# Optimization experiments

Measured on AMD Instinct MI355X. Metric: run time of the kernel, lower is better.

The kernel has to match this reference:

```python
import jax, jax.numpy as jnp
import numpy as np


def setup_inputs() -> dict:
    key = jax.random.key(0)
    k1, k2 = jax.random.split(key)
    B, T, D, K = 16, 4096, 1024, 512
    h = jax.random.normal(k1, (B, T, D), dtype=jnp.float32)
    codebook = jax.random.normal(k2, (K, D), dtype=jnp.float32)
    return {"h": h, "codebook": codebook}


def reference(h, codebook):
    """SAMMCodebook.encode: nearest-codeword indices via squared L2 distance.

    h: [B, T, D]; codebook: [K, D] -> z: [B, T] int32
    """
    B, T, D = h.shape
    h_flat = h.reshape(-1, D)                                  # [N, D]
    h_sq = jnp.sum(h_flat * h_flat, axis=-1, keepdims=True)    # [N, 1]
    c_sq = jnp.sum(codebook * codebook, axis=-1)[None, :]      # [1, K]
    # dist[n,k] = ||h_n||^2 + ||c_k||^2 - 2 <h_n, c_k>
    dist = h_sq + c_sq - 2.0 * (h_flat @ codebook.T)           # [N, K]
    z = jnp.argmin(dist, axis=-1).reshape(B, T)
    return z.astype(jnp.int32)
```

## Files before the change

### kernel.cpp

```cpp
#include <hip/hip_runtime.h>


#define D_DIM 1024
#define K_CB  512
#define BM    64
#define BN    256
#define BK    64
#define STRIDE 72
#define DELTA 4.0f
#define SENTINEL 0x7FFF

typedef __attribute__((ext_vector_type(8))) short short8;
typedef __attribute__((ext_vector_type(4))) float floatx4;

static __device__ __forceinline__ unsigned short f2bf(float f) {
    unsigned u = __builtin_bit_cast(unsigned, f);
    unsigned r = (u + 0x7FFFu + ((u >> 16) & 1u)) >> 16;
    return (unsigned short)r;
}

__global__ __launch_bounds__(256)
void prep_kernel(const float* __restrict__ cb, unsigned short* __restrict__ cbb,
                 float* __restrict__ csq) {
    __shared__ float red[4];
    const int k = blockIdx.x, t = threadIdx.x;
    const float4 v = *(const float4*)(cb + (size_t)k * D_DIM + t * 4);
    uint2 u;
    u.x = (unsigned)f2bf(v.x) | ((unsigned)f2bf(v.y) << 16);
    u.y = (unsigned)f2bf(v.z) | ((unsigned)f2bf(v.w) << 16);
    *(uint2*)(cbb + (size_t)k * D_DIM + t * 4) = u;
    float s = v.x * v.x + v.y * v.y + v.z * v.z + v.w * v.w;
    #pragma unroll
    for (int off = 32; off > 0; off >>= 1) s += __shfl_down(s, off, 64);
    if ((t & 63) == 0) red[t >> 6] = s;
    __syncthreads();
    if (t == 0) csq[k] = red[0] + red[1] + red[2] + red[3];
}

__global__ __launch_bounds__(256)
void coarse_kernel(const float* __restrict__ h,
                   const unsigned short* __restrict__ cbb,
                   const float* __restrict__ csq,
                   uint4* __restrict__ slots) {
    __shared__ unsigned char smem[46080] __attribute__((aligned(16)));
    unsigned short* hs = (unsigned short*)smem;
    unsigned short* cs = (unsigned short*)(smem + 64 * STRIDE * 2);

    const int tid = threadIdx.x;
    const int w = tid >> 6;
    const int lane = tid & 63;
    const int l15 = lane & 15;
    const int kq = lane >> 4;

    const int rowblk = blockIdx.x >> 1;
    const int half = blockIdx.x & 1;
    const size_t row0 = (size_t)rowblk * BM;
    const int col0 = half * BN;

    const int wr = (w >> 1) * 32;
    const int wc = (w & 1) * 128;

    floatx4 acc[2][8];
    #pragma unroll
    for (int i = 0; i < 2; ++i)
        #pragma unroll
        for (int j = 0; j < 8; ++j) acc[i][j] = (floatx4){0.f, 0.f, 0.f, 0.f};

    for (int dk = 0; dk < D_DIM; dk += BK) {
        #pragma unroll
        for (int p = 0; p < 4; ++p) {
            const int f = p * 256 + tid;
            const int r = f >> 4, c4 = f & 15;
            const float4 v = *(const float4*)(h + (row0 + r) * D_DIM + dk + c4 * 4);
            uint2 u;
            u.x = (unsigned)f2bf(v.x) | ((unsigned)f2bf(v.y) << 16);
            u.y = (unsigned)f2bf(v.z) | ((unsigned)f2bf(v.w) << 16);
            *(uint2*)(hs + r * STRIDE + c4 * 4) = u;
        }
        #pragma unroll
        for (int p = 0; p < 8; ++p) {
            const int f = p * 256 + tid;
            const int cr = f >> 3, g = f & 7;
            const uint4 u = *(const uint4*)(cbb + (size_t)(col0 + cr) * D_DIM + dk + g * 8);
            *(uint4*)(cs + cr * STRIDE + g * 8) = u;
        }
        __syncthreads();
        #pragma unroll
        for (int ks = 0; ks < BK; ks += 32) {
            short8 a[2], b[8];
            #pragma unroll
            for (int rt = 0; rt < 2; ++rt)
                a[rt] = *(const short8*)(hs + (wr + rt * 16 + l15) * STRIDE + ks + kq * 8);
            #pragma unroll
            for (int ct = 0; ct < 8; ++ct)
                b[ct] = *(const short8*)(cs + (wc + ct * 16 + l15) * STRIDE + ks + kq * 8);
            #pragma unroll
            for (int rt = 0; rt < 2; ++rt)
                #pragma unroll
                for (int ct = 0; ct < 8; ++ct)
                    acc[rt][ct] = __builtin_amdgcn_mfma_f32_16x16x32_bf16(
                        a[rt], b[ct], acc[rt][ct], 0, 0, 0);
        }
        __syncthreads();
    }

    float k1[8], k2[8];
    int   c1[8], c2[8];
    #pragma unroll
    for (int i = 0; i < 8; ++i) { k1[i] = 3.4e38f; k2[i] = 3.4e38f; c1[i] = 0; c2[i] = 0; }

    #pragma unroll
    for (int ct = 0; ct < 8; ++ct) {
        const int col = col0 + wc + ct * 16 + l15;
        const float cq = csq[col];
        #pragma unroll
        for (int rt = 0; rt < 2; ++rt)
            #pragma unroll
            for (int reg = 0; reg < 4; ++reg) {
                const float s = fmaf(-2.0f, acc[rt][ct][reg], cq);
                const int ri = rt * 4 + reg;
                if (s < k1[ri]) { k2[ri] = k1[ri]; c2[ri] = c1[ri]; k1[ri] = s; c1[ri] = col; }
                else if (s < k2[ri]) { k2[ri] = s; c2[ri] = col; }
            }
    }

    float* mval = (float*)smem;
    int*   mcol = (int*)(smem + 64 * 66 * 4);
    __syncthreads();
    #pragma unroll
    for (int rt = 0; rt < 2; ++rt)
        #pragma unroll
        for (int reg = 0; reg < 4; ++reg) {
            const int ri = rt * 4 + reg;
            const int r = wr + rt * 16 + kq * 4 + reg;
            const int e = ((w & 1) * 16 + l15) * 2;
            mval[r * 66 + e] = k1[ri];     mcol[r * 66 + e] = c1[ri];
            mval[r * 66 + e + 1] = k2[ri]; mcol[r * 66 + e + 1] = c2[ri];
        }
    __syncthreads();

    if (tid < 64) {
        const int r = tid;
        float bv = 3.4e38f; int bc = 0x7fffffff;
        for (int e = 0; e < 64; ++e) {
            const float v = mval[r * 66 + e];
            const int   c = mcol[r * 66 + e];
            if (v < bv || (v == bv && c < bc)) { bv = v; bc = c; }
        }
        const float thr = bv + DELTA;
        unsigned cd[4] = {0, 0, 0, 0};
        int others = 0;
        for (int e = 0; e < 64; ++e) {
            const float v = mval[r * 66 + e];
            const int   c = mcol[r * 66 + e];
            if (v < thr && c != bc) {
                if (others < 4) cd[others] = (unsigned)c;
                ++others;
            }
        }
        unsigned cnt = (others > 4) ? (unsigned)SENTINEL : (unsigned)(1 + others);
        uint4 s;
        s.x = __builtin_bit_cast(unsigned, bv);
        s.y = (unsigned)bc | (cnt << 16);
        s.z = cd[0] | (cd[1] << 16);
        s.w = cd[2] | (cd[3] << 16);
        slots[(row0 + r) * 2 + half] = s;
    }
}

__global__ __launch_bounds__(256)
void refine_kernel(const float* __restrict__ h, const float* __restrict__ cb,
                   const float* __restrict__ csq, const uint4* __restrict__ slots,
                   int* __restrict__ out) {
    const int w = threadIdx.x >> 6;
    const int lane = threadIdx.x & 63;
    const size_t row = (size_t)blockIdx.x * 4 + w;

    const uint4 s0 = slots[row * 2 + 0];
    const uint4 s1 = slots[row * 2 + 1];
    const float bv0 = __builtin_bit_cast(float, s0.x);
    const float bv1 = __builtin_bit_cast(float, s1.x);
    const float gmin = fminf(bv0, bv1);
    const float thr = gmin + DELTA;

    int cl[10];
    int nc = 0;
    bool full = false;
    {
        const uint4 ss[2] = {s0, s1};
        const float bvh[2] = {bv0, bv1};
        for (int hh = 0; hh < 2; ++hh) {
            if (!(bvh[hh] < thr)) continue;
            const unsigned cnt = ss[hh].y >> 16;
            if (cnt == SENTINEL) { full = true; continue; }
            cl[nc++] = (int)(ss[hh].y & 0xFFFFu);
            const unsigned cds[4] = {ss[hh].z & 0xFFFFu, ss[hh].z >> 16,
                                     ss[hh].w & 0xFFFFu, ss[hh].w >> 16};
            for (unsigned i = 0; i + 1 < cnt; ++i) cl[nc++] = (int)cds[i];
        }
    }

    if (!full && nc == 1) {
        if (lane == 0) out[row] = cl[0];
        return;
    }

    const float* hrow = h + row * D_DIM;
    float4 hv[4];
    #pragma unroll
    for (int j = 0; j < 4; ++j)
        hv[j] = *(const float4*)(hrow + j * 256 + lane * 4);

    float bs = 3.4e38f; int bc = 0x7fffffff;
    const int total = full ? K_CB : nc;
    for (int i = 0; i < total; ++i) {
        const int c = full ? i : cl[i];
        const float* crow = cb + (size_t)c * D_DIM;
        float d = 0.0f;
        #pragma unroll
        for (int j = 0; j < 4; ++j) {
            const float4 cv = *(const float4*)(crow + j * 256 + lane * 4);
            d = fmaf(hv[j].x, cv.x, d);
            d = fmaf(hv[j].y, cv.y, d);
            d = fmaf(hv[j].z, cv.z, d);
            d = fmaf(hv[j].w, cv.w, d);
        }
        #pragma unroll
        for (int off = 32; off > 0; off >>= 1) d += __shfl_down(d, off, 64);
        d = __shfl(d, 0, 64);
        const float s = fmaf(-2.0f, d, csq[c]);
        if (s < bs || (s == bs && c < bc)) { bs = s; bc = c; }
    }
    if (lane == 0) out[row] = bc;
}

extern "C" void kernel_launch(void* const* d_in, const int* in_sizes, int n_in,
                              void* d_out, int out_size, void* d_ws, size_t ws_size,
                              hipStream_t stream) {
    const float* h  = (const float*)d_in[0];
    const float* cb = (const float*)d_in[1];
    int* out = (int*)d_out;

    unsigned char* ws = (unsigned char*)d_ws;
    unsigned short* cbb = (unsigned short*)ws;
    float* csq = (float*)(ws + 1048576);
    uint4* slots = (uint4*)(ws + 1048576 + 2048);

    const int nrows = in_sizes[0] / D_DIM;

    prep_kernel<<<dim3(K_CB), dim3(256), 0, stream>>>(cb, cbb, csq);
    coarse_kernel<<<dim3((nrows / BM) * 2), dim3(256), 0, stream>>>(h, cbb, csq, slots);
    refine_kernel<<<dim3(nrows / 4), dim3(256), 0, stream>>>(h, cb, csq, slots, out);
}
```

Before: 486.1 us.

## Pre-convert h to bf16, async LDS-load GEMM over full codebook, worklist refine

```diff
diff --git a/kernel.cpp b/kernel.cpp
--- a/kernel.cpp
+++ b/kernel.cpp
@@ -3,20 +3,42 @@
 
 #define D_DIM 1024
 #define K_CB  512
-#define BM    64
-#define BN    256
-#define BK    64
-#define STRIDE 72
 #define DELTA 4.0f
-#define SENTINEL 0x7FFF
+#define SENTINEL 0x7FFFu
 
 typedef __attribute__((ext_vector_type(8))) short short8;
 typedef __attribute__((ext_vector_type(4))) float floatx4;
 
-static __device__ __forceinline__ unsigned short f2bf(float f) {
+#define WS_HB    0ull
+#define WS_CBB   134217728ull
+#define WS_CSQ   135266304ull
+#define WS_SLOT  135268352ull
+#define WS_WL    136316928ull
+#define WS_CNT   136579072ull
+#define WS_NEED  136579136ull
+
+typedef const unsigned int __attribute__((address_space(1)))* gaddr_t;
+typedef unsigned int __attribute__((address_space(3)))* laddr_t;
+static __device__ __forceinline__ void async_copy16(const void* g, void* l) {
+    __builtin_amdgcn_global_load_lds((gaddr_t)g, (laddr_t)l, 16, 0, 0);
+}
+
+static __device__ __forceinline__ unsigned f2bf(float f) {
     unsigned u = __builtin_bit_cast(unsigned, f);
-    unsigned r = (u + 0x7FFFu + ((u >> 16) & 1u)) >> 16;
-    return (unsigned short)r;
+    return (u + 0x7FFFu + ((u >> 16) & 1u)) >> 16;
+}
+
+__global__ __launch_bounds__(256)
+void hconv_kernel(const float* __restrict__ h, unsigned short* __restrict__ hb) {
+    const size_t i = ((size_t)blockIdx.x * 256 + threadIdx.x) * 8;
+    const float4 v0 = *(const float4*)(h + i);
+    const float4 v1 = *(const float4*)(h + i + 4);
+    uint4 u;
+    u.x = f2bf(v0.x) | (f2bf(v0.y) << 16);
+    u.y = f2bf(v0.z) | (f2bf(v0.w) << 16);
+    u.z = f2bf(v1.x) | (f2bf(v1.y) << 16);
+    u.w = f2bf(v1.z) | (f2bf(v1.w) << 16);
+    *(uint4*)(hb + i) = u;
 }
 
 __global__ __launch_bounds__(256)
@@ -26,8 +48,8 @@
     const int k = blockIdx.x, t = threadIdx.x;
     const float4 v = *(const float4*)(cb + (size_t)k * D_DIM + t * 4);
     uint2 u;
-    u.x = (unsigned)f2bf(v.x) | ((unsigned)f2bf(v.y) << 16);
-    u.y = (unsigned)f2bf(v.z) | ((unsigned)f2bf(v.w) << 16);
+    u.x = f2bf(v.x) | (f2bf(v.y) << 16);
+    u.y = f2bf(v.z) | (f2bf(v.w) << 16);
     *(uint2*)(cbb + (size_t)k * D_DIM + t * 4) = u;
     float s = v.x * v.x + v.y * v.y + v.z * v.z + v.w * v.w;
     #pragma unroll
@@ -37,6 +59,202 @@
     if (t == 0) csq[k] = red[0] + red[1] + red[2] + red[3];
 }
 
+__global__ __launch_bounds__(256, 2)
+void coarse2_kernel(const unsigned short* __restrict__ hb,
+                    const unsigned short* __restrict__ cbb,
+                    const float* __restrict__ csq,
+                    uint4* __restrict__ slots,
+                    int* __restrict__ wl,
+                    unsigned* __restrict__ wcount,
+                    int* __restrict__ out) {
+    __shared__ unsigned char smem[33792] __attribute__((aligned(16)));
+    unsigned short* As = (unsigned short*)smem;
+    unsigned short* Bs = (unsigned short*)(smem + 8192);
+
+    const int tid = threadIdx.x;
+    const int w = tid >> 6, lane = tid & 63;
+    const int l15 = lane & 15, kq = lane >> 4;
+    const int wr = (w >> 1) * 64, wc = (w & 1) * 64;
+    const size_t row0 = (size_t)blockIdx.x * 128;
+
+    int rS[2], qS[2];
+    #pragma unroll
+    for (int j = 0; j < 2; ++j) {
+        const int slot = j * 256 + w * 64 + lane;
+        rS[j] = slot >> 2; qS[j] = slot & 3;
+    }
+    const unsigned short* gA[2];
+    #pragma unroll
+    for (int j = 0; j < 2; ++j)
+        gA[j] = hb + (row0 + rS[j]) * D_DIM + qS[j] * 8;
+
+    float k1[16], k2[16];
+    unsigned cpk[16];
+    #pragma unroll
+    for (int i = 0; i < 16; ++i) { k1[i] = 3.4e38f; k2[i] = 3.4e38f; cpk[i] = 0; }
+
+    for (int cc = 0; cc < 4; ++cc) {
+        floatx4 acc[4][4];
+        #pragma unroll
+        for (int i = 0; i < 4; ++i)
+            #pragma unroll
+            for (int j = 0; j < 4; ++j) acc[i][j] = (floatx4){0.f, 0.f, 0.f, 0.f};
+
+        const unsigned short* gB[2];
+        #pragma unroll
+        for (int j = 0; j < 2; ++j)
+            gB[j] = cbb + (size_t)(cc * 128 + rS[j]) * D_DIM + qS[j] * 8;
+
+        #pragma unroll 2
+        for (int dk = 0; dk < D_DIM; dk += 32) {
+            #pragma unroll
+            for (int j = 0; j < 2; ++j) {
+                const size_t lds_off = (size_t)(j * 256 + w * 64) * 8;
+                async_copy16(gA[j] + dk, As + lds_off);
+                async_copy16(gB[j] + dk, Bs + lds_off);
+            }
+            __syncthreads();
+            short8 a[4], b[4];
+            #pragma unroll
+            for (int rt = 0; rt < 4; ++rt)
+                a[rt] = *(const short8*)(As + (wr + rt * 16 + l15) * 32 + kq * 8);
+            #pragma unroll
+            for (int ct = 0; ct < 4; ++ct)
+                b[ct] = *(const short8*)(Bs + (wc + ct * 16 + l15) * 32 + kq * 8);
+            #pragma unroll
+            for (int rt = 0; rt < 4; ++rt)
+                #pragma unroll
+                for (int ct = 0; ct < 4; ++ct)
+                    acc[rt][ct] = __builtin_amdgcn_mfma_f32_16x16x32_bf16(
+                        a[rt], b[ct], acc[rt][ct], 0, 0, 0);
+            __syncthreads();
+        }
+
+        #pragma unroll
+        for (int ct = 0; ct < 4; ++ct) {
+            const int col = cc * 128 + wc + ct * 16 + l15;
+            const float cq = csq[col];
+            #pragma unroll
+            for (int rt = 0; rt < 4; ++rt)
+                #pragma unroll
+                for (int reg = 0; reg < 4; ++reg) {
+                    const float s = fmaf(-2.0f, acc[rt][ct][reg], cq);
+                    const int ri = rt * 4 + reg;
+                    if (s < k1[ri]) {
+                        k2[ri] = k1[ri]; k1[ri] = s;
+                        cpk[ri] = (cpk[ri] << 16) | (unsigned)col;
+                    } else if (s < k2[ri]) {
+                        k2[ri] = s;
+                        cpk[ri] = (cpk[ri] & 0xFFFFu) | ((unsigned)col << 16);
+                    }
+                }
+        }
+    }
+
+    float* mval = (float*)smem;
+    int*   mcol = (int*)(smem + 16896);
+    for (int p = 0; p < 2; ++p) {
+        __syncthreads();
+        if ((w >> 1) == p) {
+            #pragma unroll
+            for (int rt = 0; rt < 4; ++rt)
+                #pragma unroll
+                for (int reg = 0; reg < 4; ++reg) {
+                    const int ri = rt * 4 + reg;
+                    const int rl = rt * 16 + kq * 4 + reg;
+                    const int e = ((w & 1) * 16 + l15) * 2;
+                    mval[rl * 66 + e] = k1[ri];
+                    mcol[rl * 66 + e] = (int)(cpk[ri] & 0xFFFFu);
+                    mval[rl * 66 + e + 1] = k2[ri];
+                    mcol[rl * 66 + e + 1] = (int)(cpk[ri] >> 16);
+                }
+        }
+        __syncthreads();
+        if (tid < 64) {
+            const int r = tid;
+            float bv = mval[r * 66]; int bc = mcol[r * 66];
+            for (int e = 1; e < 64; ++e) {
+                const float v = mval[r * 66 + e];
+                const int   c = mcol[r * 66 + e];
+                if (v < bv || (v == bv && c < bc)) { bv = v; bc = c; }
+            }
+            const float thr = bv + DELTA;
+            unsigned cd[4] = {0, 0, 0, 0};
+            int others = 0;
+            for (int e = 0; e < 64; ++e) {
+                const float v = mval[r * 66 + e];
+                const int   c = mcol[r * 66 + e];
+                if (v < thr && c != bc) {
+                    if (others < 4) cd[others] = (unsigned)c;
+                    ++others;
+                }
+            }
+            const size_t grow = row0 + (size_t)p * 64 + r;
+            if (others == 0) {
+                out[grow] = bc;
+            } else {
+                const unsigned cnt = (others > 4) ? SENTINEL : (unsigned)(1 + others);
+                uint4 s;
+                s.x = __builtin_bit_cast(unsigned, bv);
+                s.y = (unsigned)bc | (cnt << 16);
+                s.z = cd[0] | (cd[1] << 16);
+                s.w = cd[2] | (cd[3] << 16);
+                slots[grow] = s;
+                wl[atomicAdd(wcount, 1u)] = (int)grow;
+            }
+        }
+    }
+}
+
+__global__ __launch_bounds__(256)
+void refine2_kernel(const float* __restrict__ h, const float* __restrict__ cb,
+                    const float* __restrict__ csq, const uint4* __restrict__ slots,
+                    const int* __restrict__ wl, const unsigned* __restrict__ wcount,
+                    int* __restrict__ out) {
+    const int w = threadIdx.x >> 6, lane = threadIdx.x & 63;
+    const unsigned total = *wcount;
+    for (unsigned idx = blockIdx.x * 4 + w; idx < total; idx += 1024) {
+        const size_t row = (size_t)wl[idx];
+        const uint4 s = slots[row];
+        const unsigned cnt = s.y >> 16;
+        const bool full = (cnt == SENTINEL);
+        int cl[5]; int nc = 0;
+        if (!full) {
+            nc = (int)cnt;
+            cl[0] = (int)(s.y & 0xFFFFu);
+            const unsigned cds[4] = {s.z & 0xFFFFu, s.z >> 16, s.w & 0xFFFFu, s.w >> 16};
+            for (int i = 1; i < nc; ++i) cl[i] = (int)cds[i - 1];
+        }
+        const float* hrow = h + row * D_DIM;
+        float4 hv[4];
+        #pragma unroll
+        for (int j = 0; j < 4; ++j)
+            hv[j] = *(const float4*)(hrow + j * 256 + lane * 4);
+        float bs = 3.4e38f; int bc = 0x7fffffff;
+        const int tot = full ? K_CB : nc;
+        for (int i = 0; i < tot; ++i) {
+            const int c = full ? i : cl[i];
+            const float* crow = cb + (size_t)c * D_DIM;
+            float d = 0.0f;
+            #pragma unroll
+            for (int j = 0; j < 4; ++j) {
+                const float4 cv = *(const float4*)(crow + j * 256 + lane * 4);
+                d = fmaf(hv[j].x, cv.x, d);
+                d = fmaf(hv[j].y, cv.y, d);
+                d = fmaf(hv[j].z, cv.z, d);
+                d = fmaf(hv[j].w, cv.w, d);
+            }
+            #pragma unroll
+            for (int off = 32; off > 0; off >>= 1) d += __shfl_down(d, off, 64);
+            d = __shfl(d, 0, 64);
+            const float sc = fmaf(-2.0f, d, csq[c]);
+            if (sc < bs || (sc == bs && c < bc)) { bs = sc; bc = c; }
+        }
+        if (lane == 0) out[row] = bc;
+    }
+}
+
+#define STRIDE 72
 __global__ __launch_bounds__(256)
 void coarse_kernel(const float* __restrict__ h,
                    const unsigned short* __restrict__ cbb,
@@ -45,36 +263,27 @@
     __shared__ unsigned char smem[46080] __attribute__((aligned(16)));
     unsigned short* hs = (unsigned short*)smem;
     unsigned short* cs = (unsigned short*)(smem + 64 * STRIDE * 2);
-
     const int tid = threadIdx.x;
-    const int w = tid >> 6;
-    const int lane = tid & 63;
-    const int l15 = lane & 15;
-    const int kq = lane >> 4;
-
-    const int rowblk = blockIdx.x >> 1;
-    const int half = blockIdx.x & 1;
-    const size_t row0 = (size_t)rowblk * BM;
-    const int col0 = half * BN;
-
-    const int wr = (w >> 1) * 32;
-    const int wc = (w & 1) * 128;
-
+    const int w = tid >> 6, lane = tid & 63;
+    const int l15 = lane & 15, kq = lane >> 4;
+    const int rowblk = blockIdx.x >> 1, half = blockIdx.x & 1;
+    const size_t row0 = (size_t)rowblk * 64;
+    const int col0 = half * 256;
+    const int wr = (w >> 1) * 32, wc = (w & 1) * 128;
     floatx4 acc[2][8];
     #pragma unroll
     for (int i = 0; i < 2; ++i)
         #pragma unroll
         for (int j = 0; j < 8; ++j) acc[i][j] = (floatx4){0.f, 0.f, 0.f, 0.f};
-
-    for (int dk = 0; dk < D_DIM; dk += BK) {
+    for (int dk = 0; dk < D_DIM; dk += 64) {
         #pragma unroll
         for (int p = 0; p < 4; ++p) {
             const int f = p * 256 + tid;
             const int r = f >> 4, c4 = f & 15;
             const float4 v = *(const float4*)(h + (row0 + r) * D_DIM + dk + c4 * 4);
             uint2 u;
-            u.x = (unsigned)f2bf(v.x) | ((unsigned)f2bf(v.y) << 16);
-            u.y = (unsigned)f2bf(v.z) | ((unsigned)f2bf(v.w) << 16);
+            u.x = f2bf(v.x) | (f2bf(v.y) << 16);
+            u.y = f2bf(v.z) | (f2bf(v.w) << 16);
             *(uint2*)(hs + r * STRIDE + c4 * 4) = u;
         }
         #pragma unroll
@@ -86,7 +295,7 @@
         }
         __syncthreads();
         #pragma unroll
-        for (int ks = 0; ks < BK; ks += 32) {
+        for (int ks = 0; ks < 64; ks += 32) {
             short8 a[2], b[8];
             #pragma unroll
             for (int rt = 0; rt < 2; ++rt)
@@ -103,12 +312,9 @@
         }
         __syncthreads();
     }
-
-    float k1[8], k2[8];
-    int   c1[8], c2[8];
+    float k1[8], k2[8]; int c1[8], c2[8];
     #pragma unroll
     for (int i = 0; i < 8; ++i) { k1[i] = 3.4e38f; k2[i] = 3.4e38f; c1[i] = 0; c2[i] = 0; }
-
     #pragma unroll
     for (int ct = 0; ct < 8; ++ct) {
         const int col = col0 + wc + ct * 16 + l15;
@@ -123,7 +329,6 @@
                 else if (s < k2[ri]) { k2[ri] = s; c2[ri] = col; }
             }
     }
-
     float* mval = (float*)smem;
     int*   mcol = (int*)(smem + 64 * 66 * 4);
     __syncthreads();
@@ -138,7 +343,6 @@
             mval[r * 66 + e + 1] = k2[ri]; mcol[r * 66 + e + 1] = c2[ri];
         }
     __syncthreads();
-
     if (tid < 64) {
         const int r = tid;
         float bv = 3.4e38f; int bc = 0x7fffffff;
@@ -158,7 +362,7 @@
                 ++others;
             }
         }
-        unsigned cnt = (others > 4) ? (unsigned)SENTINEL : (unsigned)(1 + others);
+        unsigned cnt = (others > 4) ? SENTINEL : (unsigned)(1 + others);
         uint4 s;
         s.x = __builtin_bit_cast(unsigned, bv);
         s.y = (unsigned)bc | (cnt << 16);
@@ -172,20 +376,14 @@
 void refine_kernel(const float* __restrict__ h, const float* __restrict__ cb,
                    const float* __restrict__ csq, const uint4* __restrict__ slots,
                    int* __restrict__ out) {
-    const int w = threadIdx.x >> 6;
-    const int lane = threadIdx.x & 63;
+    const int w = threadIdx.x >> 6, lane = threadIdx.x & 63;
     const size_t row = (size_t)blockIdx.x * 4 + w;
-
     const uint4 s0 = slots[row * 2 + 0];
     const uint4 s1 = slots[row * 2 + 1];
     const float bv0 = __builtin_bit_cast(float, s0.x);
     const float bv1 = __builtin_bit_cast(float, s1.x);
-    const float gmin = fminf(bv0, bv1);
-    const float thr = gmin + DELTA;
-
-    int cl[10];
-    int nc = 0;
-    bool full = false;
+    const float thr = fminf(bv0, bv1) + DELTA;
+    int cl[10]; int nc = 0; bool full = false;
     {
         const uint4 ss[2] = {s0, s1};
         const float bvh[2] = {bv0, bv1};
@@ -199,18 +397,11 @@
             for (unsigned i = 0; i + 1 < cnt; ++i) cl[nc++] = (int)cds[i];
         }
     }
-
-    if (!full && nc == 1) {
-        if (lane == 0) out[row] = cl[0];
-        return;
-    }
-
+    if (!full && nc == 1) { if (lane == 0) out[row] = cl[0]; return; }
     const float* hrow = h + row * D_DIM;
     float4 hv[4];
     #pragma unroll
-    for (int j = 0; j < 4; ++j)
-        hv[j] = *(const float4*)(hrow + j * 256 + lane * 4);
-
+    for (int j = 0; j < 4; ++j) hv[j] = *(const float4*)(hrow + j * 256 + lane * 4);
     float bs = 3.4e38f; int bc = 0x7fffffff;
     const int total = full ? K_CB : nc;
     for (int i = 0; i < total; ++i) {
@@ -228,8 +419,8 @@
         #pragma unroll
         for (int off = 32; off > 0; off >>= 1) d += __shfl_down(d, off, 64);
         d = __shfl(d, 0, 64);
-        const float s = fmaf(-2.0f, d, csq[c]);
-        if (s < bs || (s == bs && c < bc)) { bs = s; bc = c; }
+        const float sc = fmaf(-2.0f, d, csq[c]);
+        if (sc < bs || (sc == bs && c < bc)) { bs = sc; bc = c; }
     }
     if (lane == 0) out[row] = bc;
 }
@@ -240,15 +431,29 @@
     const float* h  = (const float*)d_in[0];
     const float* cb = (const float*)d_in[1];
     int* out = (int*)d_out;
-
     unsigned char* ws = (unsigned char*)d_ws;
-    unsigned short* cbb = (unsigned short*)ws;
-    float* csq = (float*)(ws + 1048576);
-    uint4* slots = (uint4*)(ws + 1048576 + 2048);
-
     const int nrows = in_sizes[0] / D_DIM;
 
-    prep_kernel<<<dim3(K_CB), dim3(256), 0, stream>>>(cb, cbb, csq);
-    coarse_kernel<<<dim3((nrows / BM) * 2), dim3(256), 0, stream>>>(h, cbb, csq, slots);
-    refine_kernel<<<dim3(nrows / 4), dim3(256), 0, stream>>>(h, cb, csq, slots, out);
-}
+    if (ws_size >= WS_NEED) {
+        unsigned short* hb  = (unsigned short*)(ws + WS_HB);
+        unsigned short* cbb = (unsigned short*)(ws + WS_CBB);
+        float* csq   = (float*)(ws + WS_CSQ);
+        uint4* slots = (uint4*)(ws + WS_SLOT);
+        int*   wl    = (int*)(ws + WS_WL);
+        unsigned* wc = (unsigned*)(ws + WS_CNT);
+        hipMemsetAsync(wc, 0, 4, stream);
+        hconv_kernel<<<dim3((nrows * (D_DIM / 8)) / 256), dim3(256), 0, stream>>>(h, hb);
+        prep_kernel<<<dim3(K_CB), dim3(256), 0, stream>>>(cb, cbb, csq);
+        coarse2_kernel<<<dim3(nrows / 128), dim3(256), 0, stream>>>(
+            hb, cbb, csq, slots, wl, wc, out);
+        refine2_kernel<<<dim3(256), dim3(256), 0, stream>>>(
+            h, cb, csq, slots, wl, wc, out);
+    } else {
+        unsigned short* cbb = (unsigned short*)ws;
+        float* csq   = (float*)(ws + 1048576);
+        uint4* slots = (uint4*)(ws + 1048576 + 2048);
+        prep_kernel<<<dim3(K_CB), dim3(256), 0, stream>>>(cb, cbb, csq);
+        coarse_kernel<<<dim3((nrows / 64) * 2), dim3(256), 0, stream>>>(h, cbb, csq, slots);
+        refine_kernel<<<dim3(nrows / 4), dim3(256), 0, stream>>>(h, cb, csq, slots, out);
+    }
+}
```

Result: slower. 880.6 us (+81.2%).

## Cover full codebook per block, async-load B, and compact refine worklist

Applied to the files above, without the earlier changes.

```diff
diff --git a/kernel.cpp b/kernel.cpp
--- a/kernel.cpp
+++ b/kernel.cpp
@@ -3,20 +3,28 @@
 
 #define D_DIM 1024
 #define K_CB  512
-#define BM    64
-#define BN    256
-#define BK    64
-#define STRIDE 72
 #define DELTA 4.0f
-#define SENTINEL 0x7FFF
+#define MAXC  8
+#define SENT  0xFFFFu
 
 typedef __attribute__((ext_vector_type(8))) short short8;
 typedef __attribute__((ext_vector_type(4))) float floatx4;
 
-static __device__ __forceinline__ unsigned short f2bf(float f) {
+#define WS_CBB  0ull
+#define WS_CSQ  1048576ull
+#define WS_SLOT 1050624ull
+#define WS_WL   3147776ull
+#define WS_CNT  3409920ull
+
+typedef const unsigned int __attribute__((address_space(1)))* gaddr_t;
+typedef unsigned int __attribute__((address_space(3)))* laddr_t;
+static __device__ __forceinline__ void async_copy16(const void* g, void* l) {
+    __builtin_amdgcn_global_load_lds((gaddr_t)g, (laddr_t)l, 16, 0, 0);
+}
+
+static __device__ __forceinline__ unsigned f2bf(float f) {
     unsigned u = __builtin_bit_cast(unsigned, f);
-    unsigned r = (u + 0x7FFFu + ((u >> 16) & 1u)) >> 16;
-    return (unsigned short)r;
+    return (u + 0x7FFFu + ((u >> 16) & 1u)) >> 16;
 }
 
 __global__ __launch_bounds__(256)
@@ -26,8 +34,8 @@
     const int k = blockIdx.x, t = threadIdx.x;
     const float4 v = *(const float4*)(cb + (size_t)k * D_DIM + t * 4);
     uint2 u;
-    u.x = (unsigned)f2bf(v.x) | ((unsigned)f2bf(v.y) << 16);
-    u.y = (unsigned)f2bf(v.z) | ((unsigned)f2bf(v.w) << 16);
+    u.x = f2bf(v.x) | (f2bf(v.y) << 16);
+    u.y = f2bf(v.z) | (f2bf(v.w) << 16);
     *(uint2*)(cbb + (size_t)k * D_DIM + t * 4) = u;
     float s = v.x * v.x + v.y * v.y + v.z * v.z + v.w * v.w;
     #pragma unroll
@@ -37,172 +45,168 @@
     if (t == 0) csq[k] = red[0] + red[1] + red[2] + red[3];
 }
 
-__global__ __launch_bounds__(256)
+__global__ __launch_bounds__(256, 2)
 void coarse_kernel(const float* __restrict__ h,
                    const unsigned short* __restrict__ cbb,
                    const float* __restrict__ csq,
-                   uint4* __restrict__ slots) {
-    __shared__ unsigned char smem[46080] __attribute__((aligned(16)));
-    unsigned short* hs = (unsigned short*)smem;
-    unsigned short* cs = (unsigned short*)(smem + 64 * STRIDE * 2);
+                   uint4* __restrict__ slots,
+                   int* __restrict__ wl,
+                   unsigned* __restrict__ wcount,
+                   int* __restrict__ out) {
+    __shared__ unsigned char smem[66560] __attribute__((aligned(16)));
+    unsigned short* As = (unsigned short*)smem;
+    unsigned short* Bs = (unsigned short*)(smem + 4096);
 
     const int tid = threadIdx.x;
-    const int w = tid >> 6;
-    const int lane = tid & 63;
-    const int l15 = lane & 15;
-    const int kq = lane >> 4;
-
-    const int rowblk = blockIdx.x >> 1;
-    const int half = blockIdx.x & 1;
-    const size_t row0 = (size_t)rowblk * BM;
-    const int col0 = half * BN;
-
-    const int wr = (w >> 1) * 32;
-    const int wc = (w & 1) * 128;
-
-    floatx4 acc[2][8];
-    #pragma unroll
-    for (int i = 0; i < 2; ++i)
+    const int w = tid >> 6, lane = tid & 63;
+    const int l15 = lane & 15, kq = lane >> 4;
+    const size_t row0 = (size_t)blockIdx.x * 64;
+    const int wc_ = w * 128;
+
+    const int ar = tid >> 2, adq = (tid & 3) * 8;
+    const float* gA = h + (row0 + ar) * D_DIM + adq;
+    const unsigned short* gB0 = cbb + (size_t)(tid >> 2) * D_DIM + (tid & 3) * 8;
+    unsigned short* ldsB0 = Bs + (size_t)(w * 64 + (lane)) * 0;
+
+    floatx4 acc[4][8];
+    #pragma unroll
+    for (int i = 0; i < 4; ++i)
         #pragma unroll
         for (int j = 0; j < 8; ++j) acc[i][j] = (floatx4){0.f, 0.f, 0.f, 0.f};
 
-    for (int dk = 0; dk < D_DIM; dk += BK) {
-        #pragma unroll
-        for (int p = 0; p < 4; ++p) {
-            const int f = p * 256 + tid;
-            const int r = f >> 4, c4 = f & 15;
-            const float4 v = *(const float4*)(h + (row0 + r) * D_DIM + dk + c4 * 4);
-            uint2 u;
-            u.x = (unsigned)f2bf(v.x) | ((unsigned)f2bf(v.y) << 16);
-            u.y = (unsigned)f2bf(v.z) | ((unsigned)f2bf(v.w) << 16);
-            *(uint2*)(hs + r * STRIDE + c4 * 4) = u;
-        }
-        #pragma unroll
-        for (int p = 0; p < 8; ++p) {
-            const int f = p * 256 + tid;
-            const int cr = f >> 3, g = f & 7;
-            const uint4 u = *(const uint4*)(cbb + (size_t)(col0 + cr) * D_DIM + dk + g * 8);
-            *(uint4*)(cs + cr * STRIDE + g * 8) = u;
-        }
+    for (int dk = 0; dk < D_DIM; dk += 32) {
+        #pragma unroll
+        for (int j = 0; j < 8; ++j)
+            async_copy16(gB0 + (size_t)j * 64 * D_DIM + dk,
+                         Bs + (size_t)(j * 256 + w * 64) * 8);
+        const float4 v0 = *(const float4*)(gA + dk);
+        const float4 v1 = *(const float4*)(gA + dk + 4);
+        uint4 u;
+        u.x = f2bf(v0.x) | (f2bf(v0.y) << 16);
+        u.y = f2bf(v0.z) | (f2bf(v0.w) << 16);
+        u.z = f2bf(v1.x) | (f2bf(v1.y) << 16);
+        u.w = f2bf(v1.z) | (f2bf(v1.w) << 16);
+        *(uint4*)(As + ar * 32 + adq) = u;
         __syncthreads();
-        #pragma unroll
-        for (int ks = 0; ks < BK; ks += 32) {
-            short8 a[2], b[8];
-            #pragma unroll
-            for (int rt = 0; rt < 2; ++rt)
-                a[rt] = *(const short8*)(hs + (wr + rt * 16 + l15) * STRIDE + ks + kq * 8);
+
+        short8 a[4], b[8];
+        #pragma unroll
+        for (int rt = 0; rt < 4; ++rt)
+            a[rt] = *(const short8*)(As + (rt * 16 + l15) * 32 + kq * 8);
+        #pragma unroll
+        for (int ct = 0; ct < 8; ++ct)
+            b[ct] = *(const short8*)(Bs + (wc_ + ct * 16 + l15) * 32 + kq * 8);
+        #pragma unroll
+        for (int rt = 0; rt < 4; ++rt)
             #pragma unroll
             for (int ct = 0; ct < 8; ++ct)
-                b[ct] = *(const short8*)(cs + (wc + ct * 16 + l15) * STRIDE + ks + kq * 8);
-            #pragma unroll
-            for (int rt = 0; rt < 2; ++rt)
-                #pragma unroll
-                for (int ct = 0; ct < 8; ++ct)
-                    acc[rt][ct] = __builtin_amdgcn_mfma_f32_16x16x32_bf16(
-                        a[rt], b[ct], acc[rt][ct], 0, 0, 0);
-        }
+                acc[rt][ct] = __builtin_amdgcn_mfma_f32_16x16x32_bf16(
+                    a[rt], b[ct], acc[rt][ct], 0, 0, 0);
         __syncthreads();
     }
 
-    float k1[8], k2[8];
-    int   c1[8], c2[8];
-    #pragma unroll
-    for (int i = 0; i < 8; ++i) { k1[i] = 3.4e38f; k2[i] = 3.4e38f; c1[i] = 0; c2[i] = 0; }
-
+    float k1[16], k2[16];
+    unsigned cpk[16];
+    #pragma unroll
+    for (int i = 0; i < 16; ++i) { k1[i] = 3.4e38f; k2[i] = 3.4e38f; cpk[i] = 0; }
     #pragma unroll
     for (int ct = 0; ct < 8; ++ct) {
-        const int col = col0 + wc + ct * 16 + l15;
+        const int col = wc_ + ct * 16 + l15;
         const float cq = csq[col];
         #pragma unroll
-        for (int rt = 0; rt < 2; ++rt)
+        for (int rt = 0; rt < 4; ++rt)
             #pragma unroll
             for (int reg = 0; reg < 4; ++reg) {
                 const float s = fmaf(-2.0f, acc[rt][ct][reg], cq);
                 const int ri = rt * 4 + reg;
-                if (s < k1[ri]) { k2[ri] = k1[ri]; c2[ri] = c1[ri]; k1[ri] = s; c1[ri] = col; }
-                else if (s < k2[ri]) { k2[ri] = s; c2[ri] = col; }
+                if (s < k1[ri]) {
+                    k2[ri] = k1[ri]; k1[ri] = s;
+                    cpk[ri] = (cpk[ri] << 16) | (unsigned)col;
+                } else if (s < k2[ri]) {
+                    k2[ri] = s;
+                    cpk[ri] = (cpk[ri] & 0xFFFFu) | ((unsigned)col << 16);
+                }
             }
     }
 
     float* mval = (float*)smem;
-    int*   mcol = (int*)(smem + 64 * 66 * 4);
+    int*   mcol = (int*)(smem + 33280);
     __syncthreads();
     #pragma unroll
-    for (int rt = 0; rt < 2; ++rt)
+    for (int rt = 0; rt < 4; ++rt)
         #pragma unroll
         for (int reg = 0; reg < 4; ++reg) {
             const int ri = rt * 4 + reg;
-            const int r = wr + rt * 16 + kq * 4 + reg;
-            const int e = ((w & 1) * 16 + l15) * 2;
-            mval[r * 66 + e] = k1[ri];     mcol[r * 66 + e] = c1[ri];
-            mval[r * 66 + e + 1] = k2[ri]; mcol[r * 66 + e + 1] = c2[ri];
+            const int r = rt * 16 + kq * 4 + reg;
+            const int e = (w * 16 + l15) * 2;
+            mval[r * 130 + e] = k1[ri];
+            mcol[r * 130 + e] = (int)(cpk[ri] & 0xFFFFu);
+            mval[r * 130 + e + 1] = k2[ri];
+            mcol[r * 130 + e + 1] = (int)(cpk[ri] >> 16);
         }
     __syncthreads();
 
     if (tid < 64) {
         const int r = tid;
-        float bv = 3.4e38f; int bc = 0x7fffffff;
-        for (int e = 0; e < 64; ++e) {
-            const float v = mval[r * 66 + e];
-            const int   c = mcol[r * 66 + e];
+        float bv = mval[r * 130]; int bc = mcol[r * 130];
+        for (int e = 1; e < 128; ++e) {
+            const float v = mval[r * 130 + e];
+            const int   c = mcol[r * 130 + e];
             if (v < bv || (v == bv && c < bc)) { bv = v; bc = c; }
         }
         const float thr = bv + DELTA;
-        unsigned cd[4] = {0, 0, 0, 0};
+        unsigned cd[MAXC] = {0, 0, 0, 0, 0, 0, 0, 0};
         int others = 0;
-        for (int e = 0; e < 64; ++e) {
-            const float v = mval[r * 66 + e];
-            const int   c = mcol[r * 66 + e];
+        for (int e = 0; e < 128; ++e) {
+            const float v = mval[r * 130 + e];
+            const int   c = mcol[r * 130 + e];
             if (v < thr && c != bc) {
-                if (others < 4) cd[others] = (unsigned)c;
+                if (others < MAXC) cd[others] = (unsigned)c;
                 ++others;
             }
         }
-        unsigned cnt = (others > 4) ? (unsigned)SENTINEL : (unsigned)(1 + others);
-        uint4 s;
-        s.x = __builtin_bit_cast(unsigned, bv);
-        s.y = (unsigned)bc | (cnt << 16);
-        s.z = cd[0] | (cd[1] << 16);
-        s.w = cd[2] | (cd[3] << 16);
-        slots[(row0 + r) * 2 + half] = s;
+        const size_t grow = row0 + r;
+        if (others == 0) {
+            out[grow] = bc;
+        } else {
+            const unsigned cnt = (others > MAXC) ? SENT : (unsigned)others;
+            uint4 s0, s1;
+            s0.x = __builtin_bit_cast(unsigned, bv);
+            s0.y = (unsigned)bc | (cnt << 16);
+            s0.z = cd[0] | (cd[1] << 16);
+            s0.w = cd[2] | (cd[3] << 16);
+            s1.x = cd[4] | (cd[5] << 16);
+            s1.y = cd[6] | (cd[7] << 16);
+            s1.z = 0; s1.w = 0;
+            slots[grow * 2] = s0;
+            slots[grow * 2 + 1] = s1;
+            wl[atomicAdd(wcount, 1u)] = (int)grow;
+        }
     }
 }
 
 __global__ __launch_bounds__(256)
-void refine_kernel(const float* __restrict__ h, const float* __restrict__ cb,
-                   const float* __restrict__ csq, const uint4* __restrict__ slots,
-                   int* __restrict__ out) {
-    const int w = threadIdx.x >> 6;
-    const int lane = threadIdx.x & 63;
-    const size_t row = (size_t)blockIdx.x * 4 + w;
-
-    const uint4 s0 = slots[row * 2 + 0];
+void fixup_kernel(const float* __restrict__ h, const float* __restrict__ cb,
+                  const float* __restrict__ csq, const uint4* __restrict__ slots,
+                  const int* __restrict__ wl, const unsigned* __restrict__ wcount,
+                  int* __restrict__ out) {
+    const int w = threadIdx.x >> 6, lane = threadIdx.x & 63;
+    const unsigned idx = blockIdx.x * 4 + w;
+    if (idx >= *wcount) return;
+    const size_t row = (size_t)wl[idx];
+    const uint4 s0 = slots[row * 2];
     const uint4 s1 = slots[row * 2 + 1];
-    const float bv0 = __builtin_bit_cast(float, s0.x);
-    const float bv1 = __builtin_bit_cast(float, s1.x);
-    const float gmin = fminf(bv0, bv1);
-    const float thr = gmin + DELTA;
-
-    int cl[10];
-    int nc = 0;
-    bool full = false;
-    {
-        const uint4 ss[2] = {s0, s1};
-        const float bvh[2] = {bv0, bv1};
-        for (int hh = 0; hh < 2; ++hh) {
-            if (!(bvh[hh] < thr)) continue;
-            const unsigned cnt = ss[hh].y >> 16;
-            if (cnt == SENTINEL) { full = true; continue; }
-            cl[nc++] = (int)(ss[hh].y & 0xFFFFu);
-            const unsigned cds[4] = {ss[hh].z & 0xFFFFu, ss[hh].z >> 16,
-                                     ss[hh].w & 0xFFFFu, ss[hh].w >> 16};
-            for (unsigned i = 0; i + 1 < cnt; ++i) cl[nc++] = (int)cds[i];
-        }
-    }
-
-    if (!full && nc == 1) {
-        if (lane == 0) out[row] = cl[0];
-        return;
+    const unsigned cnt = s0.y >> 16;
+    const bool full = (cnt == SENT);
+    int cl[1 + MAXC]; int nc = 0;
+    if (!full) {
+        cl[0] = (int)(s0.y & 0xFFFFu);
+        const unsigned cds[MAXC] = {s0.z & 0xFFFFu, s0.z >> 16, s0.w & 0xFFFFu, s0.w >> 16,
+                                    s1.x & 0xFFFFu, s1.x >> 16, s1.y & 0xFFFFu, s1.y >> 16};
+        nc = 1 + (int)cnt;
+        #pragma unroll
+        for (int i = 0; i < MAXC; ++i)
+            if (i < (int)cnt) cl[1 + i] = (int)cds[i];
     }
 
     const float* hrow = h + row * D_DIM;
@@ -228,8 +232,8 @@
         #pragma unroll
         for (int off = 32; off > 0; off >>= 1) d += __shfl_down(d, off, 64);
         d = __shfl(d, 0, 64);
-        const float s = fmaf(-2.0f, d, csq[c]);
-        if (s < bs || (s == bs && c < bc)) { bs = s; bc = c; }
+        const float sc = fmaf(-2.0f, d, csq[c]);
+        if (sc < bs || (sc == bs && c < bc)) { bs = sc; bc = c; }
     }
     if (lane == 0) out[row] = bc;
 }
@@ -240,15 +244,19 @@
     const float* h  = (const float*)d_in[0];
     const float* cb = (const float*)d_in[1];
     int* out = (int*)d_out;
-
     unsigned char* ws = (unsigned char*)d_ws;
-    unsigned short* cbb = (unsigned short*)ws;
-    float* csq = (float*)(ws + 1048576);
-    uint4* slots = (uint4*)(ws + 1048576 + 2048);
-
     const int nrows = in_sizes[0] / D_DIM;
 
+    unsigned short* cbb = (unsigned short*)(ws + WS_CBB);
+    float* csq   = (float*)(ws + WS_CSQ);
+    uint4* slots = (uint4*)(ws + WS_SLOT);
+    int*   wl    = (int*)(ws + WS_WL);
+    unsigned* wc = (unsigned*)(ws + WS_CNT);
+
+    hipMemsetAsync(wc, 0, 4, stream);
     prep_kernel<<<dim3(K_CB), dim3(256), 0, stream>>>(cb, cbb, csq);
-    coarse_kernel<<<dim3((nrows / BM) * 2), dim3(256), 0, stream>>>(h, cbb, csq, slots);
-    refine_kernel<<<dim3(nrows / 4), dim3(256), 0, stream>>>(h, cb, csq, slots, out);
-}
+    coarse_kernel<<<dim3(nrows / 64), dim3(256), 0, stream>>>(
+        h, cbb, csq, slots, wl, wc, out);
+    fixup_kernel<<<dim3(nrows / 4), dim3(256), 0, stream>>>(
+        h, cb, csq, slots, wl, wc, out);
+}
```

Result: no change. 482.2 us (-0.8%).
